# Kernel tuning notes

Hardware: AMD Instinct MI355X
Metric: run time of the kernel (lower is better)

Reference implementation:

```python
import jax, jax.numpy as jnp
import numpy as np

PATCH_SIDE = 20  # hardcoded in GenericCamera.project


def _resize_ac(img, out_h, out_w):
    """Bilinear resize with align_corners=True, matching F.interpolate. img: (B,C,H,W)."""
    B, C, H, W = img.shape
    ys = jnp.arange(out_h, dtype=jnp.float32) * (np.float32(H - 1) / np.float32(out_h - 1))
    xs = jnp.arange(out_w, dtype=jnp.float32) * (np.float32(W - 1) / np.float32(out_w - 1))
    y0 = jnp.floor(ys).astype(jnp.int32); y1 = jnp.minimum(y0 + 1, H - 1)
    x0 = jnp.floor(xs).astype(jnp.int32); x1 = jnp.minimum(x0 + 1, W - 1)
    wy = (ys - y0.astype(jnp.float32)).astype(img.dtype)
    wx = (xs - x0.astype(jnp.float32)).astype(img.dtype)
    top = img[:, :, y0, :] * (1 - wy)[None, None, :, None] + img[:, :, y1, :] * wy[None, None, :, None]
    return top[:, :, :, x0] * (1 - wx) + top[:, :, :, x1] * wx


def setup_inputs() -> dict:
    key = jax.random.key(0)
    k1, k2 = jax.random.split(key)
    B, H, W = 1, 128, 416
    R = jax.random.normal(k1, (B, 3, H, W), dtype=jnp.float32)
    X = jax.random.normal(k2, (B, 3, H, W), dtype=jnp.float32)
    return {"R": R, "X": X, "progress": 10}


def reference(R, X, progress):
    B, C, H_full, W_full = X.shape
    kh = PATCH_SIDE
    Ks = 2 * kh + 1          # 41
    K = Ks * Ks              # 1681
    H, W = H_full // 2, W_full // 2  # downsample=True

    ray = _resize_ac(R, H, W)          # (1,3,H,W)
    direction = _resize_ac(X, H, W)    # (1,3,H,W)

    # clamped patch window start per row/col (boundary shift logic of _get_patch_coords)
    sx = jnp.clip(jnp.arange(H) - kh, 0, H - 1 - 2 * kh)   # (H,)
    sy = jnp.clip(jnp.arange(W) - kh, 0, W - 1 - 2 * kh)   # (W,)
    off = jnp.arange(Ks)
    cx = sx[:, None] + off[None, :]    # (H,41) row indices of patch
    cy = sy[:, None] + off[None, :]    # (W,41) col indices of patch

    # separable patch gather: (3,H,W) -> (3,H,41,W) -> (3,H,41,W,41)
    r = ray[0]
    patch = r[:, cx, :][:, :, :, cy]                       # (3,H,41,W,41)
    patch = patch.transpose(0, 1, 3, 2, 4).reshape(3, H * W, K)  # (3,N,K)

    dirn = direction.reshape(B, 3, H * W)
    dirn = dirn / jnp.linalg.norm(dirn, axis=1, keepdims=True)
    d = dirn[0]                                            # (3,N)

    logits = jnp.einsum('cn,cnk->nk', d, patch)            # (N,K)
    temperature = np.float32(max(1e-8, 1e-4 / np.exp(0.1 * float(progress))))
    sm = jax.nn.softmax(logits / temperature, axis=-1)     # (N,K)

    # soft-argmax over patch coordinates (coords stored as (x,y) = (row,col))
    px = jnp.broadcast_to(cx[:, None, :, None], (H, W, Ks, Ks)).reshape(H * W, K).astype(jnp.float32)
    py = jnp.broadcast_to(cy[None, :, None, :], (H, W, Ks, Ks)).reshape(H * W, K).astype(jnp.float32)
    ix = jnp.einsum('nk,nk->n', sm, px).reshape(H, W)
    iy = jnp.einsum('nk,nk->n', sm, py).reshape(H, W)

    Xn = 2.0 * ix / (H - 1) - 1.0
    Yn = 2.0 * iy / (W - 1) - 1.0
    Xn = _resize_ac(Xn[None, None], H_full, W_full)[0, 0]
    Yn = _resize_ac(Yn[None, None], H_full, W_full)[0, 0]
    return jnp.stack([Yn, Xn], axis=-1).reshape(B, H_full, W_full, 2)
```

## Files before the change

### kernel.cpp

```cpp
#include <hip/hip_runtime.h>
#include <math.h>

#define HS 64
#define WS 208
#define HF 128
#define WF 416
#define NS (HS * WS)
#define KH 20
#define KS 41
#define KK (KS * KS)
#define TW 8
#define TH 8
#define NBX (WS / TW)
#define NBY (HS / TH)
#define NBLK (NBX * NBY)
#define TDIM 48
#define LOG2E 1.442695040888963f

__device__ __forceinline__ void ac_idx(int o, int inN, float sc, int& i0, int& i1, float& w) {
#pragma clang fp contract(off)
    float s = (float)o * sc;
    float f = floorf(s);
    i0 = (int)f;
    i1 = min(i0 + 1, inN - 1);
    w = s - f;
}

__global__ __launch_bounds__(512, 1) void k_fused(const float* __restrict__ R,
                                                  const float* __restrict__ X,
                                                  const int* __restrict__ prog,
                                                  float* __restrict__ xn,
                                                  float* __restrict__ yn) {
#pragma clang fp contract(off)
    __shared__ float4 tile[TDIM * TDIM];
    __shared__ float4 dirs[64];
    __shared__ float smax_l[8][64];
    __shared__ float ssum_l[3][8][64];
    __shared__ float Tsh;

    int t = (int)threadIdx.x;
    int blk = (int)blockIdx.x;
    int by = blk / NBX, bx = blk - by * NBX;
    int ph0 = by * TH, pw0 = bx * TW;
    int srow_min = min(max(ph0 - KH, 0), HS - 1 - 2 * KH);
    int scol_min = min(max(pw0 - KH, 0), WS - 1 - 2 * KH);

    for (int e = t; e < TDIM * TDIM; e += 512) {
        int i = e / TDIM, j = e - i * TDIM;
        int g = srow_min + i, cg = scol_min + j;
        if (g < HS && cg < WS) {
            int y0, y1, x0, x1; float wy, wx;
            ac_idx(g, HF, 127.0f / 63.0f, y0, y1, wy);
            ac_idx(cg, WF, 415.0f / 207.0f, x0, x1, wx);
            float omwy = 1.0f - wy, omwx = 1.0f - wx;
            float r[3];
#pragma unroll
            for (int c = 0; c < 3; ++c) {
                const float* p = R + c * (HF * WF);
                float v00 = p[y0 * WF + x0], v10 = p[y1 * WF + x0];
                float v01 = p[y0 * WF + x1], v11 = p[y1 * WF + x1];
                float a0 = v00 * omwy; float b0 = v10 * wy; float t0 = a0 + b0;
                float a1 = v01 * omwy; float b1 = v11 * wy; float t1 = a1 + b1;
                float c0 = t0 * omwx; float c1 = t1 * wx;
                r[c] = c0 + c1;
            }
            tile[i * TDIM + (j ^ (i & 7))] = make_float4(r[0], r[1], r[2], 0.0f);
        }
    }
    if (t < 64) {
        int py = t >> 3, px = t & 7;
        int h = ph0 + py, w = pw0 + px;
        int y0, y1, x0, x1; float wy, wx;
        ac_idx(h, HF, 127.0f / 63.0f, y0, y1, wy);
        ac_idx(w, WF, 415.0f / 207.0f, x0, x1, wx);
        float omwy = 1.0f - wy, omwx = 1.0f - wx;
        float d[3];
#pragma unroll
        for (int c = 0; c < 3; ++c) {
            const float* q = X + c * (HF * WF);
            float u00 = q[y0 * WF + x0], u10 = q[y1 * WF + x0];
            float u01 = q[y0 * WF + x1], u11 = q[y1 * WF + x1];
            float e0 = u00 * omwy; float f0 = u10 * wy; float s0 = e0 + f0;
            float e1 = u01 * omwy; float f1 = u11 * wy; float s1 = e1 + f1;
            float g0 = s0 * omwx; float g1 = s1 * wx;
            d[c] = g0 + g1;
        }
        float q0 = d[0] * d[0]; float q1 = d[1] * d[1]; float q2 = d[2] * d[2];
        float ssq = (q0 + q1) + q2;
        float nrm = (float)sqrt((double)ssq);
        dirs[t] = make_float4(d[0] / nrm, d[1] / nrm, d[2] / nrm, 0.0f);
    }
    if (t == 0) {
        double T64 = fmax(1e-8, 1e-4 / exp(0.1 * (double)prog[0]));
        Tsh = (float)T64;
    }
    __syncthreads();

    int p = t & 63, s = t >> 6;
    int py = p >> 3, px = p & 7;
    int h = ph0 + py, w = pw0 + px;
    int srow = min(max(h - KH, 0), HS - 1 - 2 * KH);
    int scol = min(max(w - KH, 0), WS - 1 - 2 * KH);
    int I0 = srow - srow_min;
    int J0 = scol - scol_min;
    float4 dv = dirs[p];
    float d0 = dv.x, d1 = dv.y, d2 = dv.z;
    float Tf = Tsh;

    float m = -INFINITY;
    unsigned mask[8] = {0u, 0u, 0u, 0u, 0u, 0u, 0u, 0u};
#pragma unroll
    for (int q = 0; q < 5; ++q) {
        int r = s + 8 * q;
        int I = I0 + r;
        int rowb = I * TDIM;
        int ib = I & 7;
#pragma unroll
        for (int c = 0; c < KS; ++c) {
            float4 v = tile[rowb + ((J0 + c) ^ ib)];
            float p0 = d0 * v.x; float p1 = d1 * v.y; float p2 = d2 * v.z;
            float l = (p0 + p1) + p2;
            int ei = q * KS + c;
            bool f = l > (m - 0.004f);
            mask[ei >> 5] |= f ? (1u << (ei & 31)) : 0u;
            m = fmaxf(m, l);
        }
    }
    if (s == 0) {
        int I = I0 + 40;
        int rowb = I * TDIM;
        int ib = I & 7;
#pragma unroll
        for (int c = 0; c < KS; ++c) {
            float4 v = tile[rowb + ((J0 + c) ^ ib)];
            float p0 = d0 * v.x; float p1 = d1 * v.y; float p2 = d2 * v.z;
            float l = (p0 + p1) + p2;
            int ei = 5 * KS + c;
            bool f = l > (m - 0.004f);
            mask[ei >> 5] |= f ? (1u << (ei & 31)) : 0u;
            m = fmaxf(m, l);
        }
    }

    smax_l[s][p] = m;
    __syncthreads();
    float mf = smax_l[0][p];
#pragma unroll
    for (int s2 = 1; s2 < 8; ++s2) mf = fmaxf(mf, smax_l[s2][p]);

    float zm = mf / Tf;
    float thresh = mf - 0.004f;

    float se = 0.f, sr = 0.f, sc = 0.f;
#pragma unroll
    for (int u = 0; u < 8; ++u) {
        unsigned w8 = mask[u];
        while (w8) {
            int b = __ffs(w8) - 1;
            w8 &= w8 - 1;
            int ei = u * 32 + b;
            int q = (ei * 25) >> 10;
            int c = ei - q * KS;
            int r = s + 8 * q;
            int I = I0 + r;
            float4 v = tile[I * TDIM + ((J0 + c) ^ (I & 7))];
            float p0 = d0 * v.x; float p1 = d1 * v.y; float p2 = d2 * v.z;
            float l = (p0 + p1) + p2;
            if (l > thresh) {
                float z = l / Tf;
                float e2 = __builtin_amdgcn_exp2f((z - zm) * LOG2E);
                se += e2;
                sr += e2 * (float)(srow + r);
                sc += e2 * (float)(scol + c);
            }
        }
    }
    ssum_l[0][s][p] = se; ssum_l[1][s][p] = sr; ssum_l[2][s][p] = sc;
    __syncthreads();
    if (t < 64) {
        float SE = 0.f, SR = 0.f, SC = 0.f;
#pragma unroll
        for (int s2 = 0; s2 < 8; ++s2) {
            SE += ssum_l[0][s2][t];
            SR += ssum_l[1][s2][t];
            SC += ssum_l[2][s2][t];
        }
        int pix = (ph0 + (t >> 3)) * WS + (pw0 + (t & 7));
        double ix = (double)SR / (double)SE, iy = (double)SC / (double)SE;
        xn[pix] = (float)(2.0 * ix / (double)(HS - 1) - 1.0);
        yn[pix] = (float)(2.0 * iy / (double)(WS - 1) - 1.0);
    }
}

__global__ void k_up(const float* __restrict__ xn, const float* __restrict__ yn,
                     float* __restrict__ out) {
#pragma clang fp contract(off)
    int i = blockIdx.x * blockDim.x + threadIdx.x;
    if (i >= HF * WF) return;
    int hh = i / WF, ww = i - hh * WF;
    int y0, y1, x0, x1; float wy, wx;
    ac_idx(hh, HS, 63.0f / 127.0f, y0, y1, wy);
    ac_idx(ww, WS, 207.0f / 415.0f, x0, x1, wx);
    float omwy = 1.0f - wy, omwx = 1.0f - wx;
    float a0, b0, t0, t1;
    a0 = xn[y0 * WS + x0] * omwy; b0 = xn[y1 * WS + x0] * wy; t0 = a0 + b0;
    a0 = xn[y0 * WS + x1] * omwy; b0 = xn[y1 * WS + x1] * wy; t1 = a0 + b0;
    float bx = t0 * omwx + t1 * wx;
    a0 = yn[y0 * WS + x0] * omwy; b0 = yn[y1 * WS + x0] * wy; t0 = a0 + b0;
    a0 = yn[y0 * WS + x1] * omwy; b0 = yn[y1 * WS + x1] * wy; t1 = a0 + b0;
    float ay = t0 * omwx + t1 * wx;
    out[2 * i]     = ay;
    out[2 * i + 1] = bx;
}

extern "C" void kernel_launch(void* const* d_in, const int* in_sizes, int n_in,
                              void* d_out, int out_size, void* d_ws, size_t ws_size,
                              hipStream_t stream) {
    const float* R = (const float*)d_in[0];
    const float* X = (const float*)d_in[1];
    const int* prog = (const int*)d_in[2];
    float* xn = (float*)d_ws;
    float* yn = xn + NS;
    float* out = (float*)d_out;

    k_fused<<<NBLK, 512, 0, stream>>>(R, X, prog, xn, yn);
    k_up<<<(HF * WF + 255) / 256, 256, 0, stream>>>(xn, yn, out);
}
```

Measured before the change: 28.08 us.

## Halve pixel tile height, split patch rows over 16 slices, use padded pitch

Each block now covers a 4x8 pixel tile instead of 8x8, doubling the block count. The 512 threads are split into 16 row-slices per pixel rather than 8, which cuts the per-thread logit loop from about 5 patch rows to 3. Partial results are combined within a wave using a shuffle before the shared-memory reduction. The XOR-swizzled shared tile is replaced with a 44-row tile at padded pitch 49, and launch bounds allow 4 blocks per CU. The cost is more redundant resize work per output pixel, because the halo is now large relative to the tile, and bank conflicts may change under the new pitch.

```diff
diff --git a/kernel.cpp b/kernel.cpp
--- a/kernel.cpp
+++ b/kernel.cpp
@@ -10,11 +10,13 @@
 #define KS 41
 #define KK (KS * KS)
 #define TW 8
-#define TH 8
+#define TH 4
 #define NBX (WS / TW)
 #define NBY (HS / TH)
 #define NBLK (NBX * NBY)
-#define TDIM 48
+#define TROW 44
+#define TCOL 48
+#define PITCH 49
 #define LOG2E 1.442695040888963f
 
 __device__ __forceinline__ void ac_idx(int o, int inN, float sc, int& i0, int& i1, float& w) {
@@ -26,27 +28,29 @@
     w = s - f;
 }
 
-__global__ __launch_bounds__(512, 1) void k_fused(const float* __restrict__ R,
+__global__ __launch_bounds__(512, 4) void k_fused(const float* __restrict__ R,
                                                   const float* __restrict__ X,
                                                   const int* __restrict__ prog,
                                                   float* __restrict__ xn,
                                                   float* __restrict__ yn) {
 #pragma clang fp contract(off)
-    __shared__ float4 tile[TDIM * TDIM];
-    __shared__ float4 dirs[64];
-    __shared__ float smax_l[8][64];
-    __shared__ float ssum_l[3][8][64];
+    __shared__ float4 tile[TROW * PITCH];
+    __shared__ float4 dirs[32];
+    __shared__ float smax_l[8][32];
+    __shared__ float ssum_l[8][32][3];
     __shared__ float Tsh;
 
     int t = (int)threadIdx.x;
+    int lane = t & 63;
+    int wv = t >> 6;
     int blk = (int)blockIdx.x;
     int by = blk / NBX, bx = blk - by * NBX;
     int ph0 = by * TH, pw0 = bx * TW;
     int srow_min = min(max(ph0 - KH, 0), HS - 1 - 2 * KH);
     int scol_min = min(max(pw0 - KH, 0), WS - 1 - 2 * KH);
 
-    for (int e = t; e < TDIM * TDIM; e += 512) {
-        int i = e / TDIM, j = e - i * TDIM;
+    for (int e = t; e < TROW * TCOL; e += 512) {
+        int i = e / TCOL, j = e - i * TCOL;
         int g = srow_min + i, cg = scol_min + j;
         if (g < HS && cg < WS) {
             int y0, y1, x0, x1; float wy, wx;
@@ -64,10 +68,10 @@
                 float c0 = t0 * omwx; float c1 = t1 * wx;
                 r[c] = c0 + c1;
             }
-            tile[i * TDIM + (j ^ (i & 7))] = make_float4(r[0], r[1], r[2], 0.0f);
-        }
-    }
-    if (t < 64) {
+            tile[i * PITCH + j] = make_float4(r[0], r[1], r[2], 0.0f);
+        }
+    }
+    if (t < 32) {
         int py = t >> 3, px = t & 7;
         int h = ph0 + py, w = pw0 + px;
         int y0, y1, x0, x1; float wy, wx;
@@ -96,7 +100,7 @@
     }
     __syncthreads();
 
-    int p = t & 63, s = t >> 6;
+    int p = t & 31, s = t >> 5;
     int py = p >> 3, px = p & 7;
     int h = ph0 + py, w = pw0 + px;
     int srow = min(max(h - KH, 0), HS - 1 - 2 * KH);
@@ -108,62 +112,49 @@
     float Tf = Tsh;
 
     float m = -INFINITY;
-    unsigned mask[8] = {0u, 0u, 0u, 0u, 0u, 0u, 0u, 0u};
-#pragma unroll
-    for (int q = 0; q < 5; ++q) {
-        int r = s + 8 * q;
-        int I = I0 + r;
-        int rowb = I * TDIM;
-        int ib = I & 7;
-#pragma unroll
-        for (int c = 0; c < KS; ++c) {
-            float4 v = tile[rowb + ((J0 + c) ^ ib)];
-            float p0 = d0 * v.x; float p1 = d1 * v.y; float p2 = d2 * v.z;
-            float l = (p0 + p1) + p2;
-            int ei = q * KS + c;
-            bool f = l > (m - 0.004f);
-            mask[ei >> 5] |= f ? (1u << (ei & 31)) : 0u;
-            m = fmaxf(m, l);
-        }
-    }
-    if (s == 0) {
-        int I = I0 + 40;
-        int rowb = I * TDIM;
-        int ib = I & 7;
-#pragma unroll
-        for (int c = 0; c < KS; ++c) {
-            float4 v = tile[rowb + ((J0 + c) ^ ib)];
-            float p0 = d0 * v.x; float p1 = d1 * v.y; float p2 = d2 * v.z;
-            float l = (p0 + p1) + p2;
-            int ei = 5 * KS + c;
-            bool f = l > (m - 0.004f);
-            mask[ei >> 5] |= f ? (1u << (ei & 31)) : 0u;
-            m = fmaxf(m, l);
-        }
-    }
-
-    smax_l[s][p] = m;
+    unsigned mask[4] = {0u, 0u, 0u, 0u};
+#pragma unroll
+    for (int q = 0; q < 3; ++q) {
+        bool rv = (q < 2) || (s <= 8);
+        if (rv) {
+            int I = I0 + s + 16 * q;
+            int base = I * PITCH + J0;
+#pragma unroll
+            for (int c = 0; c < KS; ++c) {
+                float4 v = tile[base + c];
+                float p0 = d0 * v.x; float p1 = d1 * v.y; float p2 = d2 * v.z;
+                float l = (p0 + p1) + p2;
+                const int bit = q * KS + c;
+                bool f = l > (m - 0.004f);
+                mask[bit >> 5] |= f ? (1u << (bit & 31)) : 0u;
+                m = fmaxf(m, l);
+            }
+        }
+    }
+
+    m = fmaxf(m, __shfl_xor(m, 32));
+    if (lane < 32) smax_l[wv][lane] = m;
     __syncthreads();
     float mf = smax_l[0][p];
 #pragma unroll
-    for (int s2 = 1; s2 < 8; ++s2) mf = fmaxf(mf, smax_l[s2][p]);
+    for (int w2 = 1; w2 < 8; ++w2) mf = fmaxf(mf, smax_l[w2][p]);
 
     float zm = mf / Tf;
     float thresh = mf - 0.004f;
 
     float se = 0.f, sr = 0.f, sc = 0.f;
 #pragma unroll
-    for (int u = 0; u < 8; ++u) {
+    for (int u = 0; u < 4; ++u) {
         unsigned w8 = mask[u];
         while (w8) {
             int b = __ffs(w8) - 1;
             w8 &= w8 - 1;
-            int ei = u * 32 + b;
-            int q = (ei * 25) >> 10;
-            int c = ei - q * KS;
-            int r = s + 8 * q;
+            int bit = u * 32 + b;
+            int q = (bit * 25) >> 10;
+            int c = bit - q * KS;
+            int r = s + 16 * q;
             int I = I0 + r;
-            float4 v = tile[I * TDIM + ((J0 + c) ^ (I & 7))];
+            float4 v = tile[I * PITCH + J0 + c];
             float p0 = d0 * v.x; float p1 = d1 * v.y; float p2 = d2 * v.z;
             float l = (p0 + p1) + p2;
             if (l > thresh) {
@@ -175,15 +166,18 @@
             }
         }
     }
-    ssum_l[0][s][p] = se; ssum_l[1][s][p] = sr; ssum_l[2][s][p] = sc;
+    se += __shfl_xor(se, 32);
+    sr += __shfl_xor(sr, 32);
+    sc += __shfl_xor(sc, 32);
+    if (lane < 32) { ssum_l[wv][lane][0] = se; ssum_l[wv][lane][1] = sr; ssum_l[wv][lane][2] = sc; }
     __syncthreads();
-    if (t < 64) {
+    if (t < 32) {
         float SE = 0.f, SR = 0.f, SC = 0.f;
 #pragma unroll
-        for (int s2 = 0; s2 < 8; ++s2) {
-            SE += ssum_l[0][s2][t];
-            SR += ssum_l[1][s2][t];
-            SC += ssum_l[2][s2][t];
+        for (int w2 = 0; w2 < 8; ++w2) {
+            SE += ssum_l[w2][t][0];
+            SR += ssum_l[w2][t][1];
+            SC += ssum_l[w2][t][2];
         }
         int pix = (ph0 + (t >> 3)) * WS + (pw0 + (t & 7));
         double ix = (double)SR / (double)SE, iy = (double)SC / (double)SE;
```

Measured after the change: 28.60 us. Within noise of the previous version (+1.8%).
